# Optimization experiments

Measured on AMD Instinct MI355X. Metric: run time of the kernel, lower is better.

## Reference

```python
import jax, jax.numpy as jnp
import numpy as np

D_MODEL = 1024
N_HEADS = 16
HEAD_DIM = D_MODEL // N_HEADS
B, T = 4, 2048


def setup_inputs() -> dict:
    key = jax.random.key(0)
    ks = jax.random.split(key, 5)
    s = 0.02
    return {
        "x": jax.random.normal(ks[0], (B, T, D_MODEL), dtype=jnp.float32),
        "w_qkv": jax.random.normal(ks[1], (D_MODEL, 3 * D_MODEL), dtype=jnp.float32) * s,
        "b_qkv": jnp.zeros((3 * D_MODEL,), dtype=jnp.float32),
        "w_out": jax.random.normal(ks[2], (D_MODEL, D_MODEL), dtype=jnp.float32) * s,
        "b_out": jnp.zeros((D_MODEL,), dtype=jnp.float32),
    }


def reference(x, w_qkv, b_qkv, w_out, b_out):
    Bx, Tx, C = x.shape
    H, Dh = N_HEADS, HEAD_DIM
    qkv = x @ w_qkv + b_qkv                      # [B,T,3C]
    qkv = qkv.reshape(Bx, Tx, 3, H, Dh)
    q = jnp.transpose(qkv[:, :, 0], (0, 2, 1, 3))  # [B,H,T,Dh]
    k = jnp.transpose(qkv[:, :, 1], (0, 2, 1, 3))
    v = jnp.transpose(qkv[:, :, 2], (0, 2, 1, 3))
    scale = 1.0 / jnp.sqrt(jnp.asarray(Dh, dtype=x.dtype))
    attn = jnp.einsum("bhqd,bhkd->bhqk", q, k) * scale  # [B,H,T,T]
    causal = jnp.tril(jnp.ones((Tx, Tx), dtype=bool))
    attn = jnp.where(causal, attn, jnp.asarray(-jnp.inf, dtype=attn.dtype))
    attn = jax.nn.softmax(attn, axis=-1)
    out = jnp.einsum("bhqk,bhkd->bhqd", attn, v)  # [B,H,T,Dh]
    out = jnp.transpose(out, (0, 2, 1, 3)).reshape(Bx, Tx, C)
    return out @ w_out + b_out
```

## Files before the change

### kernel.cpp

```cpp
#include <hip/hip_runtime.h>
#include <hip/hip_bf16.h>
#include <stdint.h>

#define DM    1024
#define NH    16
#define DH    64
#define BATCH 4
#define SEQ   2048
#define QSCALE 0.18033688011112042f

typedef __attribute__((ext_vector_type(4))) float f32x4;
typedef __attribute__((ext_vector_type(8))) short short8;

__device__ __forceinline__ void async_load16(const void* g, void* l) {
    __builtin_amdgcn_global_load_lds(
        (const __attribute__((address_space(1))) void*)(uintptr_t)g,
        (__attribute__((address_space(3))) void*)(uintptr_t)l,
        16, 0, 0);
}

__global__ __launch_bounds__(256) void k_convert(const float* __restrict__ in,
                                                 __hip_bfloat16* __restrict__ out,
                                                 int n4, int* __restrict__ cnt) {
    if (blockIdx.x == 0 && threadIdx.x == 0) cnt[0] = 0;
    int i = blockIdx.x * 256 + threadIdx.x;
    if (i >= n4) return;
    float4 v = ((const float4*)in)[i];
    union { ushort4 u; __hip_bfloat16 h[4]; } o;
    o.h[0] = __float2bfloat16(v.x);
    o.h[1] = __float2bfloat16(v.y);
    o.h[2] = __float2bfloat16(v.z);
    o.h[3] = __float2bfloat16(v.w);
    ((ushort4*)out)[i] = o.u;
}

__global__ __launch_bounds__(256) void k_transpose(const float* __restrict__ in,
                                                   __hip_bfloat16* __restrict__ out,
                                                   int K, int N) {
    __shared__ float tile[32][33];
    const int n0 = blockIdx.x * 32, k0 = blockIdx.y * 32;
    const int tx = threadIdx.x, ty = threadIdx.y;
#pragma unroll
    for (int i = 0; i < 32; i += 8)
        tile[ty + i][tx] = in[(size_t)(k0 + ty + i) * N + n0 + tx];
    __syncthreads();
#pragma unroll
    for (int i = 0; i < 32; i += 8)
        out[(size_t)(n0 + ty + i) * K + k0 + tx] = __float2bfloat16(tile[tx][ty + i]);
}

__global__ __launch_bounds__(256) void k_gemm_qkv(
    const __hip_bfloat16* __restrict__ A, const __hip_bfloat16* __restrict__ Bt,
    const float* __restrict__ bias,
    __hip_bfloat16* __restrict__ qo, __hip_bfloat16* __restrict__ ko,
    __hip_bfloat16* __restrict__ vto) {
    constexpr int K = 1024;
    __shared__ __align__(16) __hip_bfloat16 As[128 * 64];
    __shared__ __align__(16) __hip_bfloat16 Bs[128 * 64];
    const int tid = threadIdx.x;
    const int lane = tid & 63, wid = tid >> 6;
    const int quad = lane >> 4, c = lane & 15;
    const int m0 = blockIdx.y * 128, n0 = blockIdx.x * 128;
    const int wm = (wid & 1) * 64, wn = (wid >> 1) * 64;
    f32x4 acc[4][4] = {};

    for (int k0 = 0; k0 < K; k0 += 64) {
        __syncthreads();
#pragma unroll
        for (int i = 0; i < 4; ++i) {
            const int s = tid + i * 256;
            const int r = s >> 3;
            const int g = (s & 7) ^ (r & 7);
            async_load16(A  + (size_t)(m0 + r) * K + k0 + g * 8, As + s * 8);
            async_load16(Bt + (size_t)(n0 + r) * K + k0 + g * 8, Bs + s * 8);
        }
        __syncthreads();
#pragma unroll
        for (int kk = 0; kk < 2; ++kk) {
            short8 af[4], bf[4];
#pragma unroll
            for (int mt = 0; mt < 4; ++mt) {
                const int R = wm + mt * 16 + c;
                af[mt] = *(const short8*)(As + R * 64 + (((kk * 4 + quad) ^ (R & 7)) * 8));
            }
#pragma unroll
            for (int nt = 0; nt < 4; ++nt) {
                const int R = wn + nt * 16 + c;
                bf[nt] = *(const short8*)(Bs + R * 64 + (((kk * 4 + quad) ^ (R & 7)) * 8));
            }
#pragma unroll
            for (int mt = 0; mt < 4; ++mt)
#pragma unroll
                for (int nt = 0; nt < 4; ++nt)
                    acc[mt][nt] = __builtin_amdgcn_mfma_f32_16x16x32_bf16(
                        af[mt], bf[nt], acc[mt][nt], 0, 0, 0);
        }
    }

    const int sel = n0 >> 10;
#pragma unroll
    for (int mt = 0; mt < 4; ++mt) {
        const int t0m = m0 + wm + mt * 16 + quad * 4;
        const int b = t0m >> 11, t0 = t0m & 2047;
#pragma unroll
        for (int nt = 0; nt < 4; ++nt) {
            const int n = n0 + wn + nt * 16 + c;
            const int h = (n & 1023) >> 6, dh = n & 63;
            const int bh = b * 16 + h;
            const float bv = bias[n];
            if (sel == 0) {
#pragma unroll
                for (int r = 0; r < 4; ++r)
                    qo[((size_t)bh * 2048 + t0 + r) * 64 + dh] =
                        __float2bfloat16((acc[mt][nt][r] + bv) * QSCALE);
            } else if (sel == 1) {
#pragma unroll
                for (int r = 0; r < 4; ++r)
                    ko[((size_t)bh * 2048 + t0 + r) * 64 + dh] =
                        __float2bfloat16(acc[mt][nt][r] + bv);
            } else {
                union { ushort4 u; __hip_bfloat16 hh[4]; } pk;
#pragma unroll
                for (int r = 0; r < 4; ++r)
                    pk.hh[r] = __float2bfloat16(acc[mt][nt][r] + bv);
                *(ushort4*)(vto + ((size_t)bh * 64 + dh) * 2048 + t0) = pk.u;
            }
        }
    }
}

__global__ __launch_bounds__(256) void k_attn(
    const __hip_bfloat16* __restrict__ q, const __hip_bfloat16* __restrict__ k,
    const __hip_bfloat16* __restrict__ vt, __hip_bfloat16* __restrict__ y,
    int* __restrict__ cnt) {
    __shared__ __align__(16) __hip_bfloat16 Ks[2][64 * 64];
    __shared__ __align__(16) __hip_bfloat16 Vts[2][64 * 64];
    __shared__ __align__(16) __hip_bfloat16 Ps[4][32 * 72];
    __shared__ int s_item;
    const int tid = threadIdx.x;
    const int lane = tid & 63, w = tid >> 6;
    const int quad = lane >> 4, c = lane & 15;
    __hip_bfloat16* Pw = Ps[w];
    const short one = (short)0x3F80;
    const short8 ones = {one, one, one, one, one, one, one, one};

    for (;;) {
        __syncthreads();
        if (tid == 0) s_item = atomicAdd(cnt, 1);
        __syncthreads();
        const int item = s_item;
        if (item >= 1024) break;
        const int qt = 15 - (item >> 6);
        const int bh = item & 63;
        const int b = bh >> 4, h = bh & 15;
        const int q0 = qt * 128;
        const int qw = q0 + w * 32;
        const int nkt = 2 * qt + 2;
        const size_t kbase0 = (size_t)bh * 2048 * 64;
        const size_t vbase0 = (size_t)bh * 64 * 2048;

        short8 qf[2][2];
#pragma unroll
        for (int j = 0; j < 2; ++j) {
            const __hip_bfloat16* qrow = q + ((size_t)bh * 2048 + qw + j * 16 + c) * 64;
            qf[0][j] = *(const short8*)(qrow + quad * 8);
            qf[1][j] = *(const short8*)(qrow + 32 + quad * 8);
        }

        f32x4 accO[2][4] = {};
        f32x4 accL[2] = {};

        auto stage = [&](int kt, int buf) {
#pragma unroll
            for (int i = 0; i < 2; ++i) {
                const int s = tid + i * 256;
                const int r = s >> 3;
                const int g = (s & 7) ^ (r & 7);
                async_load16(k  + kbase0 + (size_t)(kt * 64 + r) * 64 + g * 8,
                             &Ks[buf][s * 8]);
                async_load16(vt + vbase0 + (size_t)r * 2048 + kt * 64 + g * 8,
                             &Vts[buf][s * 8]);
            }
        };

        stage(0, 0);
        for (int kt = 0; kt < nkt; ++kt) {
            const int buf = kt & 1;
            __syncthreads();
            if (kt + 1 < nkt) stage(kt + 1, buf ^ 1);
            if (kt * 64 > qw + 31) continue;
            const __hip_bfloat16* Kb = Ks[buf];
            const __hip_bfloat16* Vb = Vts[buf];

            short8 kf[4][2];
#pragma unroll
            for (int nt = 0; nt < 4; ++nt) {
                const __hip_bfloat16* kr = Kb + (nt * 16 + c) * 64;
                kf[nt][0] = *(const short8*)(kr + ((quad ^ (c & 7)) * 8));
                kf[nt][1] = *(const short8*)(kr + (((quad + 4) ^ (c & 7)) * 8));
            }
            f32x4 s[2][4];
#pragma unroll
            for (int j = 0; j < 2; ++j)
#pragma unroll
                for (int nt = 0; nt < 4; ++nt) {
                    f32x4 z = {};
                    z        = __builtin_amdgcn_mfma_f32_16x16x32_bf16(kf[nt][0], qf[0][j], z, 0, 0, 0);
                    s[j][nt] = __builtin_amdgcn_mfma_f32_16x16x32_bf16(kf[nt][1], qf[1][j], z, 0, 0, 0);
                }
#pragma unroll
            for (int j = 0; j < 2; ++j) {
                if (kt * 64 + 63 > qw + j * 16) {
                    const int qg = qw + j * 16 + c;
#pragma unroll
                    for (int nt = 0; nt < 4; ++nt) {
                        const int keyb = kt * 64 + nt * 16 + quad * 4;
#pragma unroll
                        for (int r = 0; r < 4; ++r)
                            if (keyb + r > qg) s[j][nt][r] = -1e30f;
                    }
                }
            }
#pragma unroll
            for (int j = 0; j < 2; ++j)
#pragma unroll
                for (int nt = 0; nt < 4; ++nt)
#pragma unroll
                    for (int r = 0; r < 4; ++r)
                        s[j][nt][r] = exp2f(s[j][nt][r]);
#pragma unroll
            for (int j = 0; j < 2; ++j)
#pragma unroll
                for (int nt = 0; nt < 4; ++nt) {
                    union { ushort4 u4; __hip_bfloat16 hh[4]; } pk;
#pragma unroll
                    for (int r = 0; r < 4; ++r) pk.hh[r] = __float2bfloat16(s[j][nt][r]);
                    *(ushort4*)(Pw + (j * 16 + c) * 72 + nt * 16 + quad * 4) = pk.u4;
                }
            short8 pf[2][2];
#pragma unroll
            for (int j = 0; j < 2; ++j) {
                pf[0][j] = *(const short8*)(Pw + (j * 16 + c) * 72 + quad * 8);
                pf[1][j] = *(const short8*)(Pw + (j * 16 + c) * 72 + 32 + quad * 8);
            }
#pragma unroll
            for (int j = 0; j < 2; ++j) {
                accL[j] = __builtin_amdgcn_mfma_f32_16x16x32_bf16(ones, pf[0][j], accL[j], 0, 0, 0);
                accL[j] = __builtin_amdgcn_mfma_f32_16x16x32_bf16(ones, pf[1][j], accL[j], 0, 0, 0);
            }
#pragma unroll
            for (int dt = 0; dt < 4; ++dt) {
                const __hip_bfloat16* vr = Vb + (dt * 16 + c) * 64;
                short8 vf0 = *(const short8*)(vr + ((quad ^ (c & 7)) * 8));
                short8 vf1 = *(const short8*)(vr + (((quad + 4) ^ (c & 7)) * 8));
#pragma unroll
                for (int j = 0; j < 2; ++j) {
                    accO[j][dt] = __builtin_amdgcn_mfma_f32_16x16x32_bf16(vf0, pf[0][j], accO[j][dt], 0, 0, 0);
                    accO[j][dt] = __builtin_amdgcn_mfma_f32_16x16x32_bf16(vf1, pf[1][j], accO[j][dt], 0, 0, 0);
                }
            }
        }
#pragma unroll
        for (int j = 0; j < 2; ++j) {
            const float inv = 1.0f / accL[j][0];
            const int qg = qw + j * 16 + c;
#pragma unroll
            for (int dt = 0; dt < 4; ++dt) {
                union { ushort4 u; __hip_bfloat16 hh[4]; } o;
#pragma unroll
                for (int r = 0; r < 4; ++r)
                    o.hh[r] = __float2bfloat16(accO[j][dt][r] * inv);
                *(ushort4*)(y + ((size_t)b * 2048 + qg) * 1024 + h * 64 + dt * 16 + quad * 4) = o.u;
            }
        }
    }
}

__global__ __launch_bounds__(256) void k_gemm_out(
    const __hip_bfloat16* __restrict__ A, const __hip_bfloat16* __restrict__ Bt,
    const float* __restrict__ bias, float* __restrict__ out) {
    constexpr int K = 1024;
    __shared__ __align__(16) __hip_bfloat16 As[128 * 64];
    __shared__ __align__(16) __hip_bfloat16 Bs[128 * 64];
    const int tid = threadIdx.x;
    const int lane = tid & 63, wid = tid >> 6;
    const int quad = lane >> 4, c = lane & 15;
    const int m0 = blockIdx.y * 128, n0 = blockIdx.x * 128;
    const int wm = (wid & 1) * 64, wn = (wid >> 1) * 64;
    f32x4 acc[4][4] = {};

    for (int k0 = 0; k0 < K; k0 += 64) {
        __syncthreads();
#pragma unroll
        for (int i = 0; i < 4; ++i) {
            const int s = tid + i * 256;
            const int r = s >> 3;
            const int g = (s & 7) ^ (r & 7);
            async_load16(A  + (size_t)(m0 + r) * K + k0 + g * 8, As + s * 8);
            async_load16(Bt + (size_t)(n0 + r) * K + k0 + g * 8, Bs + s * 8);
        }
        __syncthreads();
#pragma unroll
        for (int kk = 0; kk < 2; ++kk) {
            short8 af[4], bf[4];
#pragma unroll
            for (int mt = 0; mt < 4; ++mt) {
                const int R = wm + mt * 16 + c;
                af[mt] = *(const short8*)(As + R * 64 + (((kk * 4 + quad) ^ (R & 7)) * 8));
            }
#pragma unroll
            for (int nt = 0; nt < 4; ++nt) {
                const int R = wn + nt * 16 + c;
                bf[nt] = *(const short8*)(Bs + R * 64 + (((kk * 4 + quad) ^ (R & 7)) * 8));
            }
#pragma unroll
            for (int mt = 0; mt < 4; ++mt)
#pragma unroll
                for (int nt = 0; nt < 4; ++nt)
                    acc[mt][nt] = __builtin_amdgcn_mfma_f32_16x16x32_bf16(
                        af[mt], bf[nt], acc[mt][nt], 0, 0, 0);
        }
    }
#pragma unroll
    for (int mt = 0; mt < 4; ++mt) {
        const int m = m0 + wm + mt * 16 + quad * 4;
#pragma unroll
        for (int nt = 0; nt < 4; ++nt) {
            const int n = n0 + wn + nt * 16 + c;
            const float bv = bias[n];
#pragma unroll
            for (int r = 0; r < 4; ++r)
                out[(size_t)(m + r) * 1024 + n] = acc[mt][nt][r] + bv;
        }
    }
}

extern "C" void kernel_launch(void* const* d_in, const int* in_sizes, int n_in,
                              void* d_out, int out_size, void* d_ws, size_t ws_size,
                              hipStream_t stream) {
    (void)in_sizes; (void)n_in; (void)out_size; (void)ws_size;
    const float* x     = (const float*)d_in[0];
    const float* w_qkv = (const float*)d_in[1];
    const float* b_qkv = (const float*)d_in[2];
    const float* w_out = (const float*)d_in[3];
    const float* b_out = (const float*)d_in[4];
    float* out = (float*)d_out;

    char* ws = (char*)d_ws;
    __hip_bfloat16* xb    = (__hip_bfloat16*)(ws + 0);
    __hip_bfloat16* wqkvT = (__hip_bfloat16*)(ws + 16777216);
    __hip_bfloat16* woutT = (__hip_bfloat16*)(ws + 23068672);
    __hip_bfloat16* qb    = (__hip_bfloat16*)(ws + 25165824);
    __hip_bfloat16* kb    = (__hip_bfloat16*)(ws + 41943040);
    __hip_bfloat16* vtb   = (__hip_bfloat16*)(ws + 58720256);
    __hip_bfloat16* yb    = (__hip_bfloat16*)(ws + 75497472);

    int* cnt = (int*)d_out;

    k_convert<<<8192, 256, 0, stream>>>(x, xb, 2097152, cnt);
    k_transpose<<<dim3(96, 32), dim3(32, 8), 0, stream>>>(w_qkv, wqkvT, 1024, 3072);
    k_transpose<<<dim3(32, 32), dim3(32, 8), 0, stream>>>(w_out, woutT, 1024, 1024);
    k_gemm_qkv<<<dim3(24, 64), 256, 0, stream>>>(xb, wqkvT, b_qkv, qb, kb, vtb);
    k_attn<<<dim3(768), 256, 0, stream>>>(qb, kb, vtb, yb, cnt);
    k_gemm_out<<<dim3(8, 64), 256, 0, stream>>>(yb, woutT, b_out, out);
}
```

Baseline: 276.5 us.

## Build attention P fragments in registers via permlane swaps instead of LDS

Removes the per-wave LDS staging buffer for the softmax probability tile. The MFMA output layout is now converted into the B-operand layout with permlane32/permlane16 swaps, and the bf16 packing uses paired conversions. It also adds s_setprio around the MFMA blocks, sets a 4-blocks-per-CU occupancy hint, and raises the persistent grid from 768 to 1024 blocks. These changes aim to cut LDS traffic and raise occupancy, at the risk of a wrong lane permutation and higher register pressure.

```diff
diff --git a/kernel.cpp b/kernel.cpp
--- a/kernel.cpp
+++ b/kernel.cpp
@@ -129,18 +129,16 @@
     }
 }
 
-__global__ __launch_bounds__(256) void k_attn(
+__global__ __launch_bounds__(256, 4) void k_attn(
     const __hip_bfloat16* __restrict__ q, const __hip_bfloat16* __restrict__ k,
     const __hip_bfloat16* __restrict__ vt, __hip_bfloat16* __restrict__ y,
     int* __restrict__ cnt) {
     __shared__ __align__(16) __hip_bfloat16 Ks[2][64 * 64];
     __shared__ __align__(16) __hip_bfloat16 Vts[2][64 * 64];
-    __shared__ __align__(16) __hip_bfloat16 Ps[4][32 * 72];
     __shared__ int s_item;
     const int tid = threadIdx.x;
     const int lane = tid & 63, w = tid >> 6;
     const int quad = lane >> 4, c = lane & 15;
-    __hip_bfloat16* Pw = Ps[w];
     const short one = (short)0x3F80;
     const short8 ones = {one, one, one, one, one, one, one, one};
 
@@ -199,17 +197,19 @@
                 kf[nt][0] = *(const short8*)(kr + ((quad ^ (c & 7)) * 8));
                 kf[nt][1] = *(const short8*)(kr + (((quad + 4) ^ (c & 7)) * 8));
             }
-            f32x4 s[2][4];
-#pragma unroll
-            for (int j = 0; j < 2; ++j)
+
+            short8 pf[2][2];
+#pragma unroll
+            for (int j = 0; j < 2; ++j) {
+                f32x4 sj[4];
+                __builtin_amdgcn_s_setprio(1);
 #pragma unroll
                 for (int nt = 0; nt < 4; ++nt) {
                     f32x4 z = {};
-                    z        = __builtin_amdgcn_mfma_f32_16x16x32_bf16(kf[nt][0], qf[0][j], z, 0, 0, 0);
-                    s[j][nt] = __builtin_amdgcn_mfma_f32_16x16x32_bf16(kf[nt][1], qf[1][j], z, 0, 0, 0);
-                }
-#pragma unroll
-            for (int j = 0; j < 2; ++j) {
+                    z      = __builtin_amdgcn_mfma_f32_16x16x32_bf16(kf[nt][0], qf[0][j], z, 0, 0, 0);
+                    sj[nt] = __builtin_amdgcn_mfma_f32_16x16x32_bf16(kf[nt][1], qf[1][j], z, 0, 0, 0);
+                }
+                __builtin_amdgcn_s_setprio(0);
                 if (kt * 64 + 63 > qw + j * 16) {
                     const int qg = qw + j * 16 + c;
 #pragma unroll
@@ -217,32 +217,39 @@
                         const int keyb = kt * 64 + nt * 16 + quad * 4;
 #pragma unroll
                         for (int r = 0; r < 4; ++r)
-                            if (keyb + r > qg) s[j][nt][r] = -1e30f;
+                            if (keyb + r > qg) sj[nt][r] = -1e30f;
                     }
                 }
-            }
-#pragma unroll
-            for (int j = 0; j < 2; ++j)
 #pragma unroll
                 for (int nt = 0; nt < 4; ++nt)
 #pragma unroll
                     for (int r = 0; r < 4; ++r)
-                        s[j][nt][r] = exp2f(s[j][nt][r]);
-#pragma unroll
-            for (int j = 0; j < 2; ++j)
+                        sj[nt][r] = exp2f(sj[nt][r]);
+                unsigned pk32[4][2];
 #pragma unroll
                 for (int nt = 0; nt < 4; ++nt) {
-                    union { ushort4 u4; __hip_bfloat16 hh[4]; } pk;
-#pragma unroll
-                    for (int r = 0; r < 4; ++r) pk.hh[r] = __float2bfloat16(s[j][nt][r]);
-                    *(ushort4*)(Pw + (j * 16 + c) * 72 + nt * 16 + quad * 4) = pk.u4;
-                }
-            short8 pf[2][2];
-#pragma unroll
-            for (int j = 0; j < 2; ++j) {
-                pf[0][j] = *(const short8*)(Pw + (j * 16 + c) * 72 + quad * 8);
-                pf[1][j] = *(const short8*)(Pw + (j * 16 + c) * 72 + 32 + quad * 8);
-            }
+                    __hip_bfloat162 lo2 = __float22bfloat162_rn(float2{sj[nt][0], sj[nt][1]});
+                    __hip_bfloat162 hi2 = __float22bfloat162_rn(float2{sj[nt][2], sj[nt][3]});
+                    pk32[nt][0] = *reinterpret_cast<unsigned*>(&lo2);
+                    pk32[nt][1] = *reinterpret_cast<unsigned*>(&hi2);
+                }
+                union U8 { unsigned u[4]; short8 v; } w0, w1;
+#pragma unroll
+                for (int rr = 0; rr < 2; ++rr) {
+                    auto t1 = __builtin_amdgcn_permlane32_swap(pk32[0][rr], pk32[1][rr], false, false);
+                    auto t2 = __builtin_amdgcn_permlane16_swap(t1[0], t1[1], false, false);
+                    w0.u[rr]     = t2[0];
+                    w0.u[2 + rr] = t2[1];
+                    t1 = __builtin_amdgcn_permlane32_swap(pk32[2][rr], pk32[3][rr], false, false);
+                    t2 = __builtin_amdgcn_permlane16_swap(t1[0], t1[1], false, false);
+                    w1.u[rr]     = t2[0];
+                    w1.u[2 + rr] = t2[1];
+                }
+                pf[0][j] = w0.v;
+                pf[1][j] = w1.v;
+            }
+
+            __builtin_amdgcn_s_setprio(1);
 #pragma unroll
             for (int j = 0; j < 2; ++j) {
                 accL[j] = __builtin_amdgcn_mfma_f32_16x16x32_bf16(ones, pf[0][j], accL[j], 0, 0, 0);
@@ -259,6 +266,7 @@
                     accO[j][dt] = __builtin_amdgcn_mfma_f32_16x16x32_bf16(vf1, pf[1][j], accO[j][dt], 0, 0, 0);
                 }
             }
+            __builtin_amdgcn_s_setprio(0);
         }
 #pragma unroll
         for (int j = 0; j < 2; ++j) {
@@ -361,6 +369,6 @@
     k_transpose<<<dim3(96, 32), dim3(32, 8), 0, stream>>>(w_qkv, wqkvT, 1024, 3072);
     k_transpose<<<dim3(32, 32), dim3(32, 8), 0, stream>>>(w_out, woutT, 1024, 1024);
     k_gemm_qkv<<<dim3(24, 64), 256, 0, stream>>>(xb, wqkvT, b_qkv, qb, kb, vtb);
-    k_attn<<<dim3(768), 256, 0, stream>>>(qb, kb, vtb, yb, cnt);
+    k_attn<<<dim3(1024), 256, 0, stream>>>(qb, kb, vtb, yb, cnt);
     k_gemm_out<<<dim3(8, 64), 256, 0, stream>>>(yb, woutT, b_out, out);
 }
```

After: 327.6 us. 1.18x slower.
